# Performance work log

Measured on AMD Instinct MI355X. Metric: run time of the kernel, lower is better.

The kernel has to match this reference:

```python
import jax, jax.numpy as jnp
import numpy as np

EMB = 1024
HEAD = 64  # emb_size // head_nb = 1024 // 16

def setup_inputs() -> dict:
    key = jax.random.key(0)
    kx, kq, kk, kv = jax.random.split(key, 4)
    x = jax.random.normal(kx, (8, 2048, EMB), dtype=jnp.float32)
    # torch nn.Linear(EMB, HEAD) weight has shape [HEAD, EMB]; y = x @ W.T
    s = 1.0 / np.sqrt(EMB)
    Wq = jax.random.uniform(kq, (HEAD, EMB), jnp.float32, -s, s)
    Wk = jax.random.uniform(kk, (HEAD, EMB), jnp.float32, -s, s)
    Wv = jax.random.uniform(kv, (HEAD, EMB), jnp.float32, -s, s)
    return {"x": x, "Wq": Wq, "Wk": Wk, "Wv": Wv}

def reference(x, Wq, Wk, Wv):
    B, T, C = x.shape
    q = jnp.einsum('btc,hc->bth', x, Wq)  # [B,T,H]
    k = jnp.einsum('btc,hc->bth', x, Wk)
    v = jnp.einsum('btc,hc->bth', x, Wv)
    scale = 1.0 / jnp.sqrt(jnp.float32(q.shape[-1]))
    wei = jnp.einsum('bth,bsh->bts', q, k) * scale  # [B,T,T]
    causal = jnp.tril(jnp.ones((T, T), dtype=bool))
    wei = jnp.where(causal, wei, -jnp.inf)
    wei = jax.nn.softmax(wei, axis=-1)
    # dropout is identity in eval mode
    out = jnp.einsum('bts,bsh->bth', wei, v)  # [B,T,H]
    return out
```

## Files before the change

### kernel.cpp

```cpp
#include <hip/hip_runtime.h>
#include <math.h>

#define SEQ  2048
#define NROW 16384
#define HEAD 64
#define EMB  1024

typedef __attribute__((ext_vector_type(8))) short short8;
typedef __attribute__((ext_vector_type(4))) float f32x4;

static __device__ __forceinline__ unsigned short f2bf(float f) {
    unsigned u = __builtin_bit_cast(unsigned, f);
    u += 0x7fffu + ((u >> 16) & 1u);
    return (unsigned short)(u >> 16);
}
static __device__ __forceinline__ float bf2f(unsigned short u) {
    unsigned v = (unsigned)u << 16;
    return __builtin_bit_cast(float, v);
}
static __device__ __forceinline__ short8 cvt8(float4 a, float4 b) {
    short8 r;
    r[0] = f2bf(a.x); r[1] = f2bf(a.y); r[2] = f2bf(a.z); r[3] = f2bf(a.w);
    r[4] = f2bf(b.x); r[5] = f2bf(b.y); r[6] = f2bf(b.z); r[7] = f2bf(b.w);
    return r;
}

__global__ __launch_bounds__(256) void wcvt_kernel(
    const float* __restrict__ Wq, const float* __restrict__ Wk,
    const float* __restrict__ Wv, unsigned short* __restrict__ Wb)
{
    const int idx = (blockIdx.x * 256 + threadIdx.x) * 4;
    const int h = idx >> 10;
    const float* src;
    if (h < 64)       src = Wq + idx;
    else if (h < 128) src = Wk + (idx - 65536);
    else              src = Wv + (idx - 131072);
    float4 f = *(const float4*)src;
    ushort4 o;
    o.x = f2bf(f.x); o.y = f2bf(f.y); o.z = f2bf(f.z); o.w = f2bf(f.w);
    *(ushort4*)(Wb + idx) = o;
}

__global__ __launch_bounds__(256, 3) void qkv_mfma_kernel(
    const float* __restrict__ x, const unsigned short* __restrict__ Wb,
    unsigned short* __restrict__ qN, unsigned short* __restrict__ kN,
    unsigned short* __restrict__ vT)
{
    __shared__ unsigned short As[2][64][72];
    __shared__ unsigned short Bs[2][96][68];

    const int tid  = threadIdx.x;
    const int w    = tid >> 6;
    const int lane = tid & 63;
    const int col  = lane & 15;
    const int quad = lane >> 4;
    const int row0 = blockIdx.x * 64;
    const int ny   = blockIdx.y;
    const int arow = w * 16 + col;

    const int sr_r = tid >> 3, sr_c = tid & 7;

    const float*          xg = x  + (size_t)(row0 + sr_r) * EMB + sr_c * 8;
    const unsigned short* bg = Wb + (size_t)(ny * 96 + sr_r) * EMB + sr_c * 8;

    short8 sa[2][2], sb[2][3];

#pragma unroll
    for (int i = 0; i < 2; ++i) {
        float4 f0 = *(const float4*)(xg + (size_t)(32 * i) * EMB);
        float4 f1 = *(const float4*)(xg + (size_t)(32 * i) * EMB + 4);
        sa[0][i] = cvt8(f0, f1);
    }
#pragma unroll
    for (int i = 0; i < 3; ++i) sb[0][i] = *(const short8*)(bg + (size_t)(32 * i) * EMB);
#pragma unroll
    for (int i = 0; i < 2; ++i) *(short8*)&As[0][sr_r + 32 * i][sr_c * 8] = sa[0][i];
#pragma unroll
    for (int i = 0; i < 3; ++i) *(short8*)&Bs[0][sr_r + 32 * i][sr_c * 8] = sb[0][i];
#pragma unroll
    for (int i = 0; i < 2; ++i) {
        float4 f0 = *(const float4*)(xg + (size_t)(32 * i) * EMB + 64);
        float4 f1 = *(const float4*)(xg + (size_t)(32 * i) * EMB + 68);
        sa[1][i] = cvt8(f0, f1);
    }
#pragma unroll
    for (int i = 0; i < 3; ++i) sb[1][i] = *(const short8*)(bg + (size_t)(32 * i) * EMB + 64);
    __syncthreads();

    f32x4 acc[6];
#pragma unroll
    for (int t = 0; t < 6; ++t) acc[t] = (f32x4){0.f, 0.f, 0.f, 0.f};

#pragma unroll
    for (int kt = 0; kt < 16; ++kt) {
        const int cur = kt & 1;
        if (kt + 2 < 16) {
            const int k0 = (kt + 2) * 64;
#pragma unroll
            for (int i = 0; i < 2; ++i) {
                float4 f0 = *(const float4*)(xg + (size_t)(32 * i) * EMB + k0);
                float4 f1 = *(const float4*)(xg + (size_t)(32 * i) * EMB + k0 + 4);
                sa[cur][i] = cvt8(f0, f1);
            }
#pragma unroll
            for (int i = 0; i < 3; ++i)
                sb[cur][i] = *(const short8*)(bg + (size_t)(32 * i) * EMB + k0);
        }
#pragma unroll
        for (int ks = 0; ks < 2; ++ks) {
            short8 af = *(const short8*)&As[cur][arow][ks * 32 + quad * 8];
#pragma unroll
            for (int t = 0; t < 6; ++t) {
                short8 bf = *(const short8*)&Bs[cur][t * 16 + col][ks * 32 + quad * 8];
                acc[t] = __builtin_amdgcn_mfma_f32_16x16x32_bf16(af, bf, acc[t], 0, 0, 0);
            }
        }
        if (kt + 1 < 16) {
#pragma unroll
            for (int i = 0; i < 2; ++i)
                *(short8*)&As[cur ^ 1][sr_r + 32 * i][sr_c * 8] = sa[cur ^ 1][i];
#pragma unroll
            for (int i = 0; i < 3; ++i)
                *(short8*)&Bs[cur ^ 1][sr_r + 32 * i][sr_c * 8] = sb[cur ^ 1][i];
        }
        __syncthreads();
    }

    const int ro = row0 + w * 16 + quad * 4;
#pragma unroll
    for (int t = 0; t < 6; ++t) {
        const int hb = ny * 96 + 16 * t;
        const int h  = hb + col;
        if (hb < 64) {
#pragma unroll
            for (int r = 0; r < 4; ++r)
                qN[(size_t)(ro + r) * HEAD + h] = f2bf(acc[t][r] * 0.125f);
        } else if (hb < 128) {
#pragma unroll
            for (int r = 0; r < 4; ++r)
                kN[(size_t)(ro + r) * HEAD + (h - 64)] = f2bf(acc[t][r]);
        } else {
            ushort4 uv;
            uv.x = f2bf(acc[t][0]); uv.y = f2bf(acc[t][1]);
            uv.z = f2bf(acc[t][2]); uv.w = f2bf(acc[t][3]);
            *(ushort4*)(vT + (size_t)(h - 128) * NROW + ro) = uv;
        }
    }
}

__global__ __launch_bounds__(256, 3) void attn_kernel(
    const unsigned short* __restrict__ qN,
    const unsigned short* __restrict__ kN,
    const unsigned short* __restrict__ vT,
    unsigned short* __restrict__ op,
    float2* __restrict__ ml)
{
    __shared__ unsigned short Ks[2][64][68];
    __shared__ unsigned short Vs[2][64][68];
    __shared__ float Pl[4][16][68];

    const int qt   = 31 - (int)blockIdx.x;
    const int b    = blockIdx.y;
    const int p    = blockIdx.z;
    const int tid  = threadIdx.x;
    const int wv   = tid >> 6;
    const int lane = tid & 63;
    const int col  = lane & 15;
    const int quad = lane >> 4;

    const int q0   = qt * 64 + wv * 16;
    const int q0g  = b * SEQ + q0;
    const int Cb   = qt + 1;
    const int kt0  = (Cb * p) >> 2;
    const int kt1  = (Cb * (p + 1)) >> 2;
    const int ktp  = min(kt0, Cb - 1);

    const int st_r = tid >> 3, st_c = tid & 7;

    const unsigned short* kg = kN + (size_t)(b * SEQ + st_r) * HEAD + st_c * 8;
    const unsigned short* vg = vT + (size_t)st_r * NROW + b * SEQ + st_c * 8;

    const short8* qp8 = (const short8*)qN + (size_t)(q0g + col) * 8;
    short8 aq0 = qp8[quad];
    short8 aq1 = qp8[quad + 4];

    f32x4 o[4];
#pragma unroll
    for (int t = 0; t < 4; ++t) o[t] = (f32x4){0.f, 0.f, 0.f, 0.f};
    float l_i[4] = {0.f, 0.f, 0.f, 0.f};

    short8 kr[2], vr[2];
#pragma unroll
    for (int i = 0; i < 2; ++i) {
        kr[i] = *(const short8*)(kg + (size_t)(ktp * 64 + 32 * i) * HEAD);
        vr[i] = *(const short8*)(vg + (size_t)(32 * i) * NROW + ktp * 64);
    }
#pragma unroll
    for (int i = 0; i < 2; ++i) {
        *(short8*)&Ks[0][st_r + 32 * i][st_c * 8] = kr[i];
        *(short8*)&Vs[0][st_r + 32 * i][st_c * 8] = vr[i];
    }
    __syncthreads();

    for (int kt = kt0; kt < kt1; ++kt) {
        const int cur = (kt - kt0) & 1;
        const int s0  = kt * 64;
        const bool diag = (kt == Cb - 1);

        if (kt + 1 < kt1) {
#pragma unroll
            for (int i = 0; i < 2; ++i) {
                kr[i] = *(const short8*)(kg + (size_t)((kt + 1) * 64 + 32 * i) * HEAD);
                vr[i] = *(const short8*)(vg + (size_t)(32 * i) * NROW + (kt + 1) * 64);
            }
        }

        f32x4 sv[4];
#pragma unroll
        for (int t = 0; t < 4; ++t) {
            short8 kf0 = *(const short8*)&Ks[cur][16 * t + col][quad * 8];
            short8 kf1 = *(const short8*)&Ks[cur][16 * t + col][32 + quad * 8];
            sv[t] = (f32x4){0.f, 0.f, 0.f, 0.f};
            sv[t] = __builtin_amdgcn_mfma_f32_16x16x32_bf16(aq0, kf0, sv[t], 0, 0, 0);
            sv[t] = __builtin_amdgcn_mfma_f32_16x16x32_bf16(aq1, kf1, sv[t], 0, 0, 0);
        }

        float pv[4][4];
#pragma unroll
        for (int r = 0; r < 4; ++r) {
            const int grow = q0 + quad * 4 + r;
#pragma unroll
            for (int t = 0; t < 4; ++t) {
                float e = __expf(sv[t][r]);
                if (diag && (s0 + 16 * t + col > grow)) e = 0.0f;
                pv[t][r] = e;
            }
            l_i[r] += (pv[0][r] + pv[1][r]) + (pv[2][r] + pv[3][r]);
        }

#pragma unroll
        for (int t = 0; t < 4; ++t)
#pragma unroll
            for (int r = 0; r < 4; ++r)
                Pl[wv][quad * 4 + r][16 * t + col] = pv[t][r];
        short8 pf[2];
#pragma unroll
        for (int st = 0; st < 2; ++st) {
            float4 pa = *(const float4*)&Pl[wv][col][quad * 8 + 32 * st];
            float4 pb = *(const float4*)&Pl[wv][col][quad * 8 + 32 * st + 4];
            pf[st] = cvt8(pa, pb);
        }

#pragma unroll
        for (int tn = 0; tn < 4; ++tn) {
            short8 vf0 = *(const short8*)&Vs[cur][16 * tn + col][quad * 8];
            short8 vf1 = *(const short8*)&Vs[cur][16 * tn + col][32 + quad * 8];
            o[tn] = __builtin_amdgcn_mfma_f32_16x16x32_bf16(pf[0], vf0, o[tn], 0, 0, 0);
            o[tn] = __builtin_amdgcn_mfma_f32_16x16x32_bf16(pf[1], vf1, o[tn], 0, 0, 0);
        }

        if (kt + 1 < kt1) {
#pragma unroll
            for (int i = 0; i < 2; ++i) {
                *(short8*)&Ks[cur ^ 1][st_r + 32 * i][st_c * 8] = kr[i];
                *(short8*)&Vs[cur ^ 1][st_r + 32 * i][st_c * 8] = vr[i];
            }
        }
        __syncthreads();
    }

#pragma unroll
    for (int r = 0; r < 4; ++r) {
        float l = l_i[r];
        l += __shfl_xor(l, 1, 16);
        l += __shfl_xor(l, 2, 16);
        l += __shfl_xor(l, 4, 16);
        l += __shfl_xor(l, 8, 16);
        l_i[r] = l;
    }
#pragma unroll
    for (int tn = 0; tn < 4; ++tn)
#pragma unroll
        for (int r = 0; r < 4; ++r)
            op[((size_t)p * NROW + q0g + quad * 4 + r) * HEAD + 16 * tn + col] =
                f2bf(o[tn][r]);
    if (col == 0) {
#pragma unroll
        for (int r = 0; r < 4; ++r)
            ml[p * NROW + q0g + quad * 4 + r] = make_float2(0.0f, l_i[r]);
    }
}

__global__ __launch_bounds__(256) void merge_kernel(
    const unsigned short* __restrict__ op, const float2* __restrict__ ml,
    float* __restrict__ out)
{
    const int idx = blockIdx.x * 256 + threadIdx.x;
    const int row = idx >> 4;
    const int hc  = (idx & 15) * 4;

    float denom = 0.0f;
#pragma unroll
    for (int p = 0; p < 4; ++p) denom += ml[p * NROW + row].y;
    const float inv = 1.0f / denom;

    float4 r = make_float4(0.f, 0.f, 0.f, 0.f);
#pragma unroll
    for (int p = 0; p < 4; ++p) {
        ushort4 u = *(const ushort4*)(op + ((size_t)p * NROW + row) * HEAD + hc);
        r.x += bf2f(u.x);
        r.y += bf2f(u.y);
        r.z += bf2f(u.z);
        r.w += bf2f(u.w);
    }
    r.x *= inv; r.y *= inv; r.z *= inv; r.w *= inv;
    *(float4*)(out + (size_t)row * HEAD + hc) = r;
}

extern "C" void kernel_launch(void* const* d_in, const int* in_sizes, int n_in,
                              void* d_out, int out_size, void* d_ws, size_t ws_size,
                              hipStream_t stream)
{
    const float* x  = (const float*)d_in[0];
    const float* Wq = (const float*)d_in[1];
    const float* Wk = (const float*)d_in[2];
    const float* Wv = (const float*)d_in[3];

    char* w = (char*)d_ws;
    unsigned short* qN = (unsigned short*)w;
    unsigned short* kN = (unsigned short*)(w + (2u << 20));
    unsigned short* vT = (unsigned short*)(w + (4u << 20));
    unsigned short* Wb = (unsigned short*)(w + (6u << 20));
    unsigned short* op = (unsigned short*)(w + (6u << 20) + 393216);
    float2*         ml = (float2*)(w + (14u << 20) + 393216);
    float* out = (float*)d_out;

    wcvt_kernel<<<192, 256, 0, stream>>>(Wq, Wk, Wv, Wb);
    qkv_mfma_kernel<<<dim3(256, 2), 256, 0, stream>>>(x, Wb, qN, kN, vT);
    attn_kernel<<<dim3(32, 8, 4), 256, 0, stream>>>(qN, kN, vT, op, ml);
    merge_kernel<<<1024, 256, 0, stream>>>(op, ml, out);
}
```

Baseline: 142.1 us.

## Load bf16 K/V and weight tiles directly into LDS with XOR-swizzled layout

Replaces the register-staged global-to-LDS copies of the weight tiles in the QKV projection, and of K/V in the attention kernel, with direct global_load_lds transfers into an unpadded, XOR-swizzled shared layout. Fragment reads are adjusted to match the swizzle. The x tile is still converted from fp32 in registers, now with a single-stage prefetch and partial unroll. This removes VGPR staging and ds_write traffic and frees registers, at the cost of relying on the async LDS load ordering and a correct swizzle for bank conflicts.

```diff
diff --git a/kernel.cpp b/kernel.cpp
--- a/kernel.cpp
+++ b/kernel.cpp
@@ -23,6 +23,17 @@
     r[0] = f2bf(a.x); r[1] = f2bf(a.y); r[2] = f2bf(a.z); r[3] = f2bf(a.w);
     r[4] = f2bf(b.x); r[5] = f2bf(b.y); r[6] = f2bf(b.z); r[7] = f2bf(b.w);
     return r;
+}
+static __device__ __forceinline__ ushort4 cvt4(float4 f) {
+    ushort4 u;
+    u.x = f2bf(f.x); u.y = f2bf(f.y); u.z = f2bf(f.z); u.w = f2bf(f.w);
+    return u;
+}
+
+static __device__ __forceinline__ void gload_lds16(const void* g, void* l) {
+    __builtin_amdgcn_global_load_lds(
+        (const __attribute__((address_space(1))) unsigned int*)g,
+        (__attribute__((address_space(3))) unsigned int*)l, 16, 0, 0);
 }
 
 __global__ __launch_bounds__(256) void wcvt_kernel(
@@ -35,10 +46,7 @@
     if (h < 64)       src = Wq + idx;
     else if (h < 128) src = Wk + (idx - 65536);
     else              src = Wv + (idx - 131072);
-    float4 f = *(const float4*)src;
-    ushort4 o;
-    o.x = f2bf(f.x); o.y = f2bf(f.y); o.z = f2bf(f.z); o.w = f2bf(f.w);
-    *(ushort4*)(Wb + idx) = o;
+    *(ushort4*)(Wb + idx) = cvt4(*(const float4*)src);
 }
 
 __global__ __launch_bounds__(256, 3) void qkv_mfma_kernel(
@@ -47,7 +55,7 @@
     unsigned short* __restrict__ vT)
 {
     __shared__ unsigned short As[2][64][72];
-    __shared__ unsigned short Bs[2][96][68];
+    __shared__ unsigned short Bs[2][96 * 64];
 
     const int tid  = threadIdx.x;
     const int w    = tid >> 6;
@@ -57,71 +65,62 @@
     const int row0 = blockIdx.x * 64;
     const int ny   = blockIdx.y;
     const int arow = w * 16 + col;
-
-    const int sr_r = tid >> 3, sr_c = tid & 7;
-
-    const float*          xg = x  + (size_t)(row0 + sr_r) * EMB + sr_c * 8;
-    const unsigned short* bg = Wb + (size_t)(ny * 96 + sr_r) * EMB + sr_c * 8;
-
-    short8 sa[2][2], sb[2][3];
-
-#pragma unroll
-    for (int i = 0; i < 2; ++i) {
-        float4 f0 = *(const float4*)(xg + (size_t)(32 * i) * EMB);
-        float4 f1 = *(const float4*)(xg + (size_t)(32 * i) * EMB + 4);
-        sa[0][i] = cvt8(f0, f1);
-    }
-#pragma unroll
-    for (int i = 0; i < 3; ++i) sb[0][i] = *(const short8*)(bg + (size_t)(32 * i) * EMB);
-#pragma unroll
-    for (int i = 0; i < 2; ++i) *(short8*)&As[0][sr_r + 32 * i][sr_c * 8] = sa[0][i];
-#pragma unroll
-    for (int i = 0; i < 3; ++i) *(short8*)&Bs[0][sr_r + 32 * i][sr_c * 8] = sb[0][i];
-#pragma unroll
-    for (int i = 0; i < 2; ++i) {
-        float4 f0 = *(const float4*)(xg + (size_t)(32 * i) * EMB + 64);
-        float4 f1 = *(const float4*)(xg + (size_t)(32 * i) * EMB + 68);
-        sa[1][i] = cvt8(f0, f1);
-    }
-#pragma unroll
-    for (int i = 0; i < 3; ++i) sb[1][i] = *(const short8*)(bg + (size_t)(32 * i) * EMB + 64);
+    const int pq   = (quad ^ (col & 7)) * 8;
+
+    const int ar_r = tid >> 4, ar_c = tid & 15;
+    const float* xg = x + (size_t)(row0 + ar_r) * EMB + ar_c * 4;
+
+    const int sr = lane >> 3, cc = (lane & 7) ^ sr;
+    const unsigned short* bg = Wb + (size_t)(ny * 96) * EMB;
+
+    {
+        float4 fa[4];
+#pragma unroll
+        for (int j = 0; j < 4; ++j) fa[j] = *(const float4*)(xg + (size_t)(16 * j) * EMB);
+#pragma unroll
+        for (int j = 0; j < 4; ++j) *(ushort4*)&As[0][ar_r + 16 * j][ar_c * 4] = cvt4(fa[j]);
+#pragma unroll
+        for (int j = 0; j < 3; ++j) {
+            const int r = (w * 3 + j) * 8 + sr;
+            gload_lds16(bg + (size_t)r * EMB + cc * 8, &Bs[0][(w * 3 + j) * 8 * 64]);
+        }
+    }
     __syncthreads();
 
     f32x4 acc[6];
 #pragma unroll
     for (int t = 0; t < 6; ++t) acc[t] = (f32x4){0.f, 0.f, 0.f, 0.f};
 
-#pragma unroll
+    float4 fa[4];
+#pragma unroll 2
     for (int kt = 0; kt < 16; ++kt) {
         const int cur = kt & 1;
-        if (kt + 2 < 16) {
-            const int k0 = (kt + 2) * 64;
-#pragma unroll
-            for (int i = 0; i < 2; ++i) {
-                float4 f0 = *(const float4*)(xg + (size_t)(32 * i) * EMB + k0);
-                float4 f1 = *(const float4*)(xg + (size_t)(32 * i) * EMB + k0 + 4);
-                sa[cur][i] = cvt8(f0, f1);
+        if (kt + 1 < 16) {
+            const int k0 = (kt + 1) * 64;
+#pragma unroll
+            for (int j = 0; j < 3; ++j) {
+                const int r = (w * 3 + j) * 8 + sr;
+                gload_lds16(bg + (size_t)r * EMB + k0 + cc * 8,
+                            &Bs[cur ^ 1][(w * 3 + j) * 8 * 64]);
             }
 #pragma unroll
-            for (int i = 0; i < 3; ++i)
-                sb[cur][i] = *(const short8*)(bg + (size_t)(32 * i) * EMB + k0);
+            for (int j = 0; j < 4; ++j)
+                fa[j] = *(const float4*)(xg + (size_t)(16 * j) * EMB + k0);
         }
 #pragma unroll
         for (int ks = 0; ks < 2; ++ks) {
             short8 af = *(const short8*)&As[cur][arow][ks * 32 + quad * 8];
+            const int po = pq ^ (ks * 32);
 #pragma unroll
             for (int t = 0; t < 6; ++t) {
-                short8 bf = *(const short8*)&Bs[cur][t * 16 + col][ks * 32 + quad * 8];
+                short8 bf = *(const short8*)&Bs[cur][(t * 16 + col) * 64 + po];
                 acc[t] = __builtin_amdgcn_mfma_f32_16x16x32_bf16(af, bf, acc[t], 0, 0, 0);
             }
         }
         if (kt + 1 < 16) {
 #pragma unroll
-            for (int i = 0; i < 2; ++i)
-                *(short8*)&As[cur ^ 1][sr_r + 32 * i][sr_c * 8] = sa[cur ^ 1][i];
-#pragma unroll
-            for (int i = 0; i < 3; ++i)
-                *(short8*)&Bs[cur ^ 1][sr_r + 32 * i][sr_c * 8] = sb[cur ^ 1][i];
+            for (int j = 0; j < 4; ++j)
+                *(ushort4*)&As[cur ^ 1][ar_r + 16 * j][ar_c * 4] = cvt4(fa[j]);
         }
         __syncthreads();
     }
@@ -155,8 +154,8 @@
     unsigned short* __restrict__ op,
     float2* __restrict__ ml)
 {
-    __shared__ unsigned short Ks[2][64][68];
-    __shared__ unsigned short Vs[2][64][68];
+    __shared__ unsigned short Ks[2][64 * 64];
+    __shared__ unsigned short Vs[2][64 * 64];
     __shared__ float Pl[4][16][68];
 
     const int qt   = 31 - (int)blockIdx.x;
@@ -175,10 +174,10 @@
     const int kt1  = (Cb * (p + 1)) >> 2;
     const int ktp  = min(kt0, Cb - 1);
 
-    const int st_r = tid >> 3, st_c = tid & 7;
-
-    const unsigned short* kg = kN + (size_t)(b * SEQ + st_r) * HEAD + st_c * 8;
-    const unsigned short* vg = vT + (size_t)st_r * NROW + b * SEQ + st_c * 8;
+    const int sr = lane >> 3, cc = (lane & 7) ^ sr;
+    const int pq = (quad ^ (col & 7)) * 8;
+    const unsigned short* kgb = kN + (size_t)(b * SEQ) * HEAD;
+    const int bcol = b * SEQ;
 
     const short8* qp8 = (const short8*)qN + (size_t)(q0g + col) * 8;
     short8 aq0 = qp8[quad];
@@ -189,16 +188,13 @@
     for (int t = 0; t < 4; ++t) o[t] = (f32x4){0.f, 0.f, 0.f, 0.f};
     float l_i[4] = {0.f, 0.f, 0.f, 0.f};
 
-    short8 kr[2], vr[2];
-#pragma unroll
-    for (int i = 0; i < 2; ++i) {
-        kr[i] = *(const short8*)(kg + (size_t)(ktp * 64 + 32 * i) * HEAD);
-        vr[i] = *(const short8*)(vg + (size_t)(32 * i) * NROW + ktp * 64);
-    }
-#pragma unroll
-    for (int i = 0; i < 2; ++i) {
-        *(short8*)&Ks[0][st_r + 32 * i][st_c * 8] = kr[i];
-        *(short8*)&Vs[0][st_r + 32 * i][st_c * 8] = vr[i];
+#pragma unroll
+    for (int j = 0; j < 2; ++j) {
+        const int r = (wv * 2 + j) * 8 + sr;
+        gload_lds16(kgb + (size_t)(ktp * 64 + r) * HEAD + cc * 8,
+                    &Ks[0][(wv * 2 + j) * 8 * 64]);
+        gload_lds16(vT + (size_t)r * NROW + bcol + ktp * 64 + cc * 8,
+                    &Vs[0][(wv * 2 + j) * 8 * 64]);
     }
     __syncthreads();
 
@@ -209,17 +205,21 @@
 
         if (kt + 1 < kt1) {
 #pragma unroll
-            for (int i = 0; i < 2; ++i) {
-                kr[i] = *(const short8*)(kg + (size_t)((kt + 1) * 64 + 32 * i) * HEAD);
-                vr[i] = *(const short8*)(vg + (size_t)(32 * i) * NROW + (kt + 1) * 64);
+            for (int j = 0; j < 2; ++j) {
+                const int r = (wv * 2 + j) * 8 + sr;
+                gload_lds16(kgb + (size_t)((kt + 1) * 64 + r) * HEAD + cc * 8,
+                            &Ks[cur ^ 1][(wv * 2 + j) * 8 * 64]);
+                gload_lds16(vT + (size_t)r * NROW + bcol + (kt + 1) * 64 + cc * 8,
+                            &Vs[cur ^ 1][(wv * 2 + j) * 8 * 64]);
             }
         }
 
         f32x4 sv[4];
 #pragma unroll
         for (int t = 0; t < 4; ++t) {
-            short8 kf0 = *(const short8*)&Ks[cur][16 * t + col][quad * 8];
-            short8 kf1 = *(const short8*)&Ks[cur][16 * t + col][32 + quad * 8];
+            const int rb = (16 * t + col) * 64;
+            short8 kf0 = *(const short8*)&Ks[cur][rb + pq];
+            short8 kf1 = *(const short8*)&Ks[cur][rb + (pq ^ 32)];
             sv[t] = (f32x4){0.f, 0.f, 0.f, 0.f};
             sv[t] = __builtin_amdgcn_mfma_f32_16x16x32_bf16(aq0, kf0, sv[t], 0, 0, 0);
             sv[t] = __builtin_amdgcn_mfma_f32_16x16x32_bf16(aq1, kf1, sv[t], 0, 0, 0);
@@ -253,19 +253,13 @@
 
 #pragma unroll
         for (int tn = 0; tn < 4; ++tn) {
-            short8 vf0 = *(const short8*)&Vs[cur][16 * tn + col][quad * 8];
-            short8 vf1 = *(const short8*)&Vs[cur][16 * tn + col][32 + quad * 8];
+            const int rb = (16 * tn + col) * 64;
+            short8 vf0 = *(const short8*)&Vs[cur][rb + pq];
+            short8 vf1 = *(const short8*)&Vs[cur][rb + (pq ^ 32)];
             o[tn] = __builtin_amdgcn_mfma_f32_16x16x32_bf16(pf[0], vf0, o[tn], 0, 0, 0);
             o[tn] = __builtin_amdgcn_mfma_f32_16x16x32_bf16(pf[1], vf1, o[tn], 0, 0, 0);
         }
 
-        if (kt + 1 < kt1) {
-#pragma unroll
-            for (int i = 0; i < 2; ++i) {
-                *(short8*)&Ks[cur ^ 1][st_r + 32 * i][st_c * 8] = kr[i];
-                *(short8*)&Vs[cur ^ 1][st_r + 32 * i][st_c * 8] = vr[i];
-            }
-        }
         __syncthreads();
     }
 
```

New measurement: 142.0 us. No clear change (-0.0%).
